# Performance work log

Hardware: AMD Instinct MI355X
Metric: run time of the kernel (lower is better)

## Reference

```python
import jax, jax.numpy as jnp
import numpy as np

B, L, DIM, HEADS, DIM_HEAD = 16, 1024, 512, 8, 64


def _make_perms(rng):
    # perm = identity on first DIM indices, random permutation of [DIM, L*DIM) after
    perms = []
    for _ in range(HEADS - 1):
        tail = rng.permutation(np.arange(DIM, L * DIM))
        perms.append(np.concatenate([np.arange(DIM), tail]))
    return jnp.asarray(np.stack(perms), dtype=jnp.int64)


def setup_inputs() -> dict:
    key = jax.random.key(0)
    ks = jax.random.split(key, 6)
    s = 0.02
    return {
        "x": jax.random.normal(ks[0], (B, L, DIM), dtype=jnp.float32),
        "perms": _make_perms(np.random.default_rng(0)),
        "Wq": jax.random.normal(ks[1], (HEADS, DIM, DIM_HEAD), dtype=jnp.float32) * s,
        "Wk": jax.random.normal(ks[2], (HEADS, DIM, DIM_HEAD), dtype=jnp.float32) * s,
        "Wv": jax.random.normal(ks[3], (HEADS, DIM, DIM_HEAD), dtype=jnp.float32) * s,
        "Wo": jax.random.normal(ks[4], (DIM, HEADS * DIM_HEAD), dtype=jnp.float32) * s,
        "bo": jnp.zeros((DIM,), dtype=jnp.float32),
    }


def reference(x, perms, Wq, Wk, Wv, Wo, bo):
    b, l, d = x.shape
    h, _, e = Wq.shape
    scale = e ** -0.5
    # shuffled query inputs for heads 1..h-1
    flat = x.reshape(b, l * d)                      # [B, L*D]
    shuf = flat[:, perms].reshape(b, h - 1, l, d)   # [B, H-1, L, D]
    xq = jnp.concatenate([x[:, None], shuf], axis=1)  # [B, H, L, D]
    q = jnp.einsum('bhld,hde->bhle', xq, Wq)
    k = jnp.einsum('bld,hde->bhle', x, Wk)
    v = jnp.einsum('bld,hde->bhle', x, Wv)
    attn = jax.nn.softmax(jnp.einsum('bhqe,bhke->bhqk', q, k) * scale, axis=-1)
    out = jnp.einsum('bhqk,bhke->bhqe', attn, v)    # [B, H, L, E]
    out = out.transpose(0, 2, 1, 3).reshape(b, l, h * e)  # concat heads on last dim
    return jnp.einsum('bli,di->bld', out, Wo) + bo
```

## Files before the change

### kernel.cpp

```cpp
#include <hip/hip_runtime.h>

#define LL 1024
#define DD 512
#define HH 8
#define EE 64
#define LDX (LL*DD)
#define BB 16

typedef _Float16 h8 __attribute__((ext_vector_type(8)));
typedef _Float16 h4 __attribute__((ext_vector_type(4)));
typedef float f4 __attribute__((ext_vector_type(4)));
typedef int i4 __attribute__((ext_vector_type(4)));

__device__ __forceinline__ f4 mfma16(h8 a, h8 b, f4 c) {
    return __builtin_amdgcn_mfma_f32_16x16x32_f16(a, b, c, 0, 0, 0);
}

__global__ __launch_bounds__(256) void k_prep(
    const float* __restrict__ x, _Float16* __restrict__ xT)
{
    const int s = blockIdx.x * 256 + threadIdx.x;
    h8 lo, hi;
    #pragma unroll
    for (int b = 0; b < 8; ++b)  lo[b] = (_Float16)x[(size_t)b*LDX + s];
    #pragma unroll
    for (int b = 0; b < 8; ++b)  hi[b] = (_Float16)x[(size_t)(b+8)*LDX + s];
    _Float16* d = xT + (size_t)s * BB;
    *(h8*)d = lo; *(h8*)(d + 8) = hi;
}

__global__ __launch_bounds__(256) void k_x16(
    const float* __restrict__ x, _Float16* __restrict__ x16)
{
    const int i = blockIdx.x * 256 + threadIdx.x;
    f4 v = ((const f4*)x)[i];
    h4 o;
    #pragma unroll
    for (int j = 0; j < 4; ++j) o[j] = (_Float16)v[j];
    *(h4*)(x16 + 4*(size_t)i) = o;
}

__global__ __launch_bounds__(256) void k_wprep(
    const float* __restrict__ Wq, const float* __restrict__ Wk,
    const float* __restrict__ Wv, _Float16* __restrict__ WT)
{
    const int d0 = blockIdx.x * 64;
    const int zz = blockIdx.y;
    const float* src; float sc = 1.f;
    if (zz < 8)       src = Wk + (size_t)zz*DD*EE;
    else if (zz < 16) src = Wv + (size_t)(zz-8)*DD*EE;
    else            { src = Wq + (size_t)(zz-16)*DD*EE; sc = 0.125f; }
    const int t = threadIdx.x;
    const int e = t & 63, dq = t >> 6;
    #pragma unroll
    for (int i = 0; i < 16; ++i) {
        int d = d0 + dq*16 + i;
        WT[(size_t)(zz*64 + e)*DD + d] = (_Float16)(src[(size_t)d*EE + e] * sc);
    }
}

__global__ __launch_bounds__(256) void k_wo16(
    const float* __restrict__ Wo, _Float16* __restrict__ Wo16)
{
    const int i = blockIdx.x * 256 + threadIdx.x;
    f4 v = ((const f4*)Wo)[i];
    #pragma unroll
    for (int j = 0; j < 4; ++j) Wo16[4*i + j] = (_Float16)v[j];
}

__global__ __launch_bounds__(256) void k_qkv(
    const _Float16* __restrict__ x16, const _Float16* __restrict__ WT,
    _Float16* __restrict__ qw, _Float16* __restrict__ kw, _Float16* __restrict__ vw)
{
    const int y  = blockIdx.x;
    const int r0 = blockIdx.y * 128;

    __shared__ __align__(16) _Float16 As[2][128][72];
    __shared__ __align__(16) _Float16 Bs[2][128][72];

    const int t = threadIdx.x;
    const int wv = t >> 6, lane = t & 63;
    const int m = lane & 15, qd = lane >> 4;
    const int sr = t >> 1, sc0 = (t & 1) * 32;

    const _Float16* ax = x16 + (size_t)(r0 + sr)*DD + sc0;
    const _Float16* bx = WT  + (size_t)(y*128 + sr)*DD + sc0;

    #pragma unroll
    for (int c = 0; c < 4; ++c) {
        *(h8*)&As[0][sr][sc0 + 8*c] = *(const h8*)(ax + 8*c);
        *(h8*)&Bs[0][sr][sc0 + 8*c] = *(const h8*)(bx + 8*c);
    }
    __syncthreads();

    f4 acc[2][8] = {};
    int cur = 0;
    for (int kt = 0; kt < 8; ++kt) {
        const int alt = cur ^ 1;
        h8 an[4], bn[4];
        if (kt < 7) {
            const _Float16* a2 = ax + (kt+1)*64;
            const _Float16* b2 = bx + (kt+1)*64;
            #pragma unroll
            for (int c = 0; c < 4; ++c) {
                an[c] = *(const h8*)(a2 + 8*c);
                bn[c] = *(const h8*)(b2 + 8*c);
            }
        }
        #pragma unroll
        for (int ks = 0; ks < 2; ++ks) {
            h8 a0 = *(const h8*)&As[cur][32*wv +  0 + m][32*ks + 8*qd];
            h8 a1 = *(const h8*)&As[cur][32*wv + 16 + m][32*ks + 8*qd];
            #pragma unroll
            for (int nt = 0; nt < 8; ++nt) {
                h8 bb = *(const h8*)&Bs[cur][16*nt + m][32*ks + 8*qd];
                acc[0][nt] = mfma16(a0, bb, acc[0][nt]);
                acc[1][nt] = mfma16(a1, bb, acc[1][nt]);
            }
        }
        if (kt < 7) {
            #pragma unroll
            for (int c = 0; c < 4; ++c) {
                *(h8*)&As[alt][sr][sc0 + 8*c] = an[c];
                *(h8*)&Bs[alt][sr][sc0 + 8*c] = bn[c];
            }
            __syncthreads();
            cur = alt;
        }
    }

    #pragma unroll
    for (int nt = 0; nt < 8; ++nt) {
        const int n = y*128 + 16*nt + m;
        const int z = n >> 6, e = n & 63;
        if (z >= 17) continue;
        _Float16* dst; int h;
        if (z < 8)       { dst = kw; h = z; }
        else if (z < 16) { dst = vw; h = z - 8; }
        else             { dst = qw; h = 0; }
        dst += (size_t)h*LL*EE + e;
        #pragma unroll
        for (int mt = 0; mt < 2; ++mt)
            #pragma unroll
            for (int r = 0; r < 4; ++r) {
                int R = r0 + 32*wv + 16*mt + 4*qd + r;
                int b = R >> 10, l = R & 1023;
                dst[((size_t)b*HH*LL + l)*EE] = (_Float16)acc[mt][nt][r];
            }
    }
}

__global__ __launch_bounds__(256) void k_qshuf(
    const _Float16* __restrict__ xT, const int* __restrict__ perms,
    const _Float16* __restrict__ WT, _Float16* __restrict__ qw)
{
    const int l0 = blockIdx.x * 4;
    const int h  = blockIdx.y + 1;
    const _Float16* Wb = WT + (size_t)((16 + h)*64)*DD;
    const int* pbase = perms + (size_t)(h-1)*LDX;

    __shared__ __align__(16) _Float16 As[2][64][72];
    __shared__ __align__(16) _Float16 Bs[2][64][72];

    const int t = threadIdx.x;
    const int wv = t >> 6, lane = t & 63;
    const int m = lane & 15, qd = lane >> 4;
    const int lg = t >> 6, kcol = t & 63;
    const int br = t >> 2, bc0 = (t & 3) * 16;

    int pv[8];
    #pragma unroll
    for (int kt = 0; kt < 8; ++kt)
        pv[kt] = pbase[(size_t)(l0 + lg)*DD + kt*64 + kcol];

    {
        const _Float16* g = xT + (size_t)pv[0] * BB;
        h8 g0 = *(const h8*)g, g1 = *(const h8*)(g + 8);
        const _Float16* s = Wb + (size_t)br*DD + bc0;
        *(h8*)&Bs[0][br][bc0]     = *(const h8*)s;
        *(h8*)&Bs[0][br][bc0 + 8] = *(const h8*)(s + 8);
        #pragma unroll
        for (int i = 0; i < 8; ++i) As[0][lg*16 + i][kcol]     = g0[i];
        #pragma unroll
        for (int i = 0; i < 8; ++i) As[0][lg*16 + 8 + i][kcol] = g1[i];
    }
    __syncthreads();

    f4 acc[4] = {};
    int cur = 0;
    for (int kt = 0; kt < 8; ++kt) {
        const int alt = cur ^ 1;
        h8 g0n, g1n, b0n, b1n;
        if (kt < 7) {
            const _Float16* g = xT + (size_t)pv[kt+1] * BB;
            g0n = *(const h8*)g; g1n = *(const h8*)(g + 8);
            const _Float16* s = Wb + (size_t)br*DD + (kt+1)*64 + bc0;
            b0n = *(const h8*)s; b1n = *(const h8*)(s + 8);
        }
        #pragma unroll
        for (int ks = 0; ks < 2; ++ks) {
            h8 a = *(const h8*)&As[cur][16*wv + m][32*ks + 8*qd];
            #pragma unroll
            for (int nt = 0; nt < 4; ++nt) {
                h8 bb = *(const h8*)&Bs[cur][16*nt + m][32*ks + 8*qd];
                acc[nt] = mfma16(a, bb, acc[nt]);
            }
        }
        if (kt < 7) {
            *(h8*)&Bs[alt][br][bc0]     = b0n;
            *(h8*)&Bs[alt][br][bc0 + 8] = b1n;
            #pragma unroll
            for (int i = 0; i < 8; ++i) As[alt][lg*16 + i][kcol]     = g0n[i];
            #pragma unroll
            for (int i = 0; i < 8; ++i) As[alt][lg*16 + 8 + i][kcol] = g1n[i];
            __syncthreads();
            cur = alt;
        }
    }
    #pragma unroll
    for (int nt = 0; nt < 4; ++nt)
        #pragma unroll
        for (int r = 0; r < 4; ++r) {
            int b = 4*qd + r;
            qw[((size_t)(b*HH + h)*LL + l0 + wv)*EE + 16*nt + m] = (_Float16)acc[nt][r];
        }
}

__global__ __launch_bounds__(256, 3) void k_attn(
    const _Float16* __restrict__ qw, const _Float16* __restrict__ kw,
    const _Float16* __restrict__ vw, _Float16* __restrict__ oa)
{
    const int bh = blockIdx.x;
    const int l0 = blockIdx.y * 128;
    const int b = bh >> 3, h = bh & 7;
    const _Float16* qb = qw + ((size_t)bh*LL + l0)*EE;
    const _Float16* kb = kw + (size_t)bh*LL*EE;
    const _Float16* vb = vw + (size_t)bh*LL*EE;

    __shared__ __align__(16) _Float16 KsF[2][64*64];
    __shared__ __align__(16) _Float16 VtsF[2][64*64];
    __shared__ __align__(16) _Float16 Ps[128][72];

    const int t = threadIdx.x;
    const int wv = t >> 6, lane = t & 63;
    const int m = lane & 15, qd = lane >> 4;
    const int m7 = m & 7;
    const int krow = t >> 2, c0 = t & 3;
    const int vkey = t & 63, vec = t >> 6;
    const int vhi = vkey >> 3, vlo = vkey & 7;

    h8 qa[2][2];
    #pragma unroll
    for (int mt = 0; mt < 2; ++mt)
        #pragma unroll
        for (int ks = 0; ks < 2; ++ks)
            qa[mt][ks] = *(const h8*)(qb + (size_t)(32*wv + 16*mt + m)*EE + 32*ks + 8*qd);

    f4 oacc[2][4] = {};
    float lp[2][4] = {};

    {
        const _Float16* sk = kb + (size_t)krow*EE + 16*c0;
        h8 k0 = *(const h8*)sk, k1 = *(const h8*)(sk + 8);
        const _Float16* sv = vb + (size_t)vkey*EE + 16*vec;
        h8 v0 = *(const h8*)sv, v1 = *(const h8*)(sv + 8);
        *(h8*)&KsF[0][(krow<<6) + 8*((2*c0)     ^ (krow & 7))] = k0;
        *(h8*)&KsF[0][(krow<<6) + 8*((2*c0 + 1) ^ (krow & 7))] = k1;
        #pragma unroll
        for (int i = 0; i < 8; ++i)
            VtsF[0][((16*vec + i)<<6)     + 8*(vhi ^ i) + vlo] = v0[i];
        #pragma unroll
        for (int i = 0; i < 8; ++i)
            VtsF[0][((16*vec + 8 + i)<<6) + 8*(vhi ^ i) + vlo] = v1[i];
    }
    __syncthreads();

    for (int kt = 0; kt < 16; ++kt) {
        const int cur = kt & 1, alt = cur ^ 1;
        h8 kn0, kn1, vn0, vn1;
        if (kt < 15) {
            const _Float16* sk = kb + (size_t)((kt+1)*64 + krow)*EE + 16*c0;
            kn0 = *(const h8*)sk; kn1 = *(const h8*)(sk + 8);
            const _Float16* sv = vb + (size_t)((kt+1)*64 + vkey)*EE + 16*vec;
            vn0 = *(const h8*)sv; vn1 = *(const h8*)(sv + 8);
        }
        f4 sacc[2][4] = {};
        #pragma unroll
        for (int ks = 0; ks < 2; ++ks)
            #pragma unroll
            for (int nt = 0; nt < 4; ++nt) {
                h8 kf = *(const h8*)&KsF[cur][((16*nt + m)<<6) + 8*((4*ks + qd) ^ m7)];
                sacc[0][nt] = mfma16(qa[0][ks], kf, sacc[0][nt]);
                sacc[1][nt] = mfma16(qa[1][ks], kf, sacc[1][nt]);
            }
        #pragma unroll
        for (int mt = 0; mt < 2; ++mt)
            #pragma unroll
            for (int nt = 0; nt < 4; ++nt)
                #pragma unroll
                for (int r = 0; r < 4; ++r) {
                    float e = __expf(sacc[mt][nt][r]);
                    lp[mt][r] += e;
                    Ps[32*wv + 16*mt + 4*qd + r][16*nt + m] = (_Float16)e;
                }
        #pragma unroll
        for (int ks = 0; ks < 2; ++ks) {
            h8 pa0 = *(const h8*)&Ps[32*wv +  0 + m][32*ks + 8*qd];
            h8 pa1 = *(const h8*)&Ps[32*wv + 16 + m][32*ks + 8*qd];
            #pragma unroll
            for (int nt = 0; nt < 4; ++nt) {
                h8 vf = *(const h8*)&VtsF[cur][((16*nt + m)<<6) + 8*((4*ks + qd) ^ m7)];
                oacc[0][nt] = mfma16(pa0, vf, oacc[0][nt]);
                oacc[1][nt] = mfma16(pa1, vf, oacc[1][nt]);
            }
        }
        if (kt < 15) {
            *(h8*)&KsF[alt][(krow<<6) + 8*((2*c0)     ^ (krow & 7))] = kn0;
            *(h8*)&KsF[alt][(krow<<6) + 8*((2*c0 + 1) ^ (krow & 7))] = kn1;
            #pragma unroll
            for (int i = 0; i < 8; ++i)
                VtsF[alt][((16*vec + i)<<6)     + 8*(vhi ^ i) + vlo] = vn0[i];
            #pragma unroll
            for (int i = 0; i < 8; ++i)
                VtsF[alt][((16*vec + 8 + i)<<6) + 8*(vhi ^ i) + vlo] = vn1[i];
            __syncthreads();
        }
    }

    #pragma unroll
    for (int mt = 0; mt < 2; ++mt)
        #pragma unroll
        for (int r = 0; r < 4; ++r) {
            float s = lp[mt][r];
            s += __shfl_xor(s, 1, 64);
            s += __shfl_xor(s, 2, 64);
            s += __shfl_xor(s, 4, 64);
            s += __shfl_xor(s, 8, 64);
            lp[mt][r] = s;
        }

    _Float16* ob = oa + ((size_t)(b*LL + l0))*(HH*EE) + h*EE;
    #pragma unroll
    for (int mt = 0; mt < 2; ++mt)
        #pragma unroll
        for (int nt = 0; nt < 4; ++nt)
            #pragma unroll
            for (int r = 0; r < 4; ++r) {
                int row = 32*wv + 16*mt + 4*qd + r;
                ob[(size_t)row*(HH*EE) + 16*nt + m] = (_Float16)(oacc[mt][nt][r] / lp[mt][r]);
            }
}

__global__ __launch_bounds__(256) void k_oproj(
    const _Float16* __restrict__ oa, const _Float16* __restrict__ Wo16,
    const float* __restrict__ bo, float* __restrict__ out)
{
    const int y  = blockIdx.x;
    const int r0 = blockIdx.y * 128;

    __shared__ __align__(16) _Float16 As[2][128][72];
    __shared__ __align__(16) _Float16 Bs[2][128][72];

    const int t = threadIdx.x;
    const int wv = t >> 6, lane = t & 63;
    const int m = lane & 15, qd = lane >> 4;
    const int sr = t >> 1, sc0 = (t & 1) * 32;

    const _Float16* ax = oa   + (size_t)(r0 + sr)*DD + sc0;
    const _Float16* bx = Wo16 + (size_t)(y*128 + sr)*DD + sc0;

    #pragma unroll
    for (int c = 0; c < 4; ++c) {
        *(h8*)&As[0][sr][sc0 + 8*c] = *(const h8*)(ax + 8*c);
        *(h8*)&Bs[0][sr][sc0 + 8*c] = *(const h8*)(bx + 8*c);
    }
    __syncthreads();

    f4 acc[2][8] = {};
    int cur = 0;
    for (int kt = 0; kt < 8; ++kt) {
        const int alt = cur ^ 1;
        h8 an[4], bn[4];
        if (kt < 7) {
            const _Float16* a2 = ax + (kt+1)*64;
            const _Float16* b2 = bx + (kt+1)*64;
            #pragma unroll
            for (int c = 0; c < 4; ++c) {
                an[c] = *(const h8*)(a2 + 8*c);
                bn[c] = *(const h8*)(b2 + 8*c);
            }
        }
        #pragma unroll
        for (int ks = 0; ks < 2; ++ks) {
            h8 a0 = *(const h8*)&As[cur][32*wv +  0 + m][32*ks + 8*qd];
            h8 a1 = *(const h8*)&As[cur][32*wv + 16 + m][32*ks + 8*qd];
            #pragma unroll
            for (int nt = 0; nt < 8; ++nt) {
                h8 bb = *(const h8*)&Bs[cur][16*nt + m][32*ks + 8*qd];
                acc[0][nt] = mfma16(a0, bb, acc[0][nt]);
                acc[1][nt] = mfma16(a1, bb, acc[1][nt]);
            }
        }
        if (kt < 7) {
            #pragma unroll
            for (int c = 0; c < 4; ++c) {
                *(h8*)&As[alt][sr][sc0 + 8*c] = an[c];
                *(h8*)&Bs[alt][sr][sc0 + 8*c] = bn[c];
            }
            __syncthreads();
            cur = alt;
        }
    }

    #pragma unroll
    for (int nt = 0; nt < 8; ++nt) {
        const int col = y*128 + 16*nt + m;
        const float bias = bo[col];
        #pragma unroll
        for (int mt = 0; mt < 2; ++mt)
            #pragma unroll
            for (int r = 0; r < 4; ++r) {
                int row = 32*wv + 16*mt + 4*qd + r;
                out[(size_t)(r0 + row)*DD + col] = acc[mt][nt][r] + bias;
            }
    }
}

extern "C" void kernel_launch(void* const* d_in, const int* in_sizes, int n_in,
                              void* d_out, int out_size, void* d_ws, size_t ws_size,
                              hipStream_t stream)
{
    const float* x  = (const float*)d_in[0];
    const int*   pm = (const int*)d_in[1];
    const float* Wq = (const float*)d_in[2];
    const float* Wk = (const float*)d_in[3];
    const float* Wv = (const float*)d_in[4];
    const float* Wo = (const float*)d_in[5];
    const float* bo = (const float*)d_in[6];
    float* out = (float*)d_out;

    const size_t QS = (size_t)BB * HH * LL * EE;
    _Float16* q    = (_Float16*)d_ws;
    _Float16* k    = q + QS;
    _Float16* v    = k + QS;
    _Float16* oaw  = v + QS;
    _Float16* xT   = oaw;
    _Float16* WT   = oaw + QS;
    _Float16* Wo16 = WT + (size_t)24*64*DD;
    _Float16* x16  = (_Float16*)d_out;

    k_x16  <<<dim3(LDX*BB/1024),    256, 0, stream>>>(x, x16);
    k_prep <<<dim3(LDX/256),        256, 0, stream>>>(x, xT);
    k_wprep<<<dim3(8, 24),          256, 0, stream>>>(Wq, Wk, Wv, WT);
    k_wo16 <<<dim3(DD*DD/1024),     256, 0, stream>>>(Wo, Wo16);
    k_qkv  <<<dim3(9, BB*LL/128),   256, 0, stream>>>(x16, WT, q, k, v);
    k_qshuf<<<dim3(LL/4, HH-1),     256, 0, stream>>>(xT, pm, WT, q);
    k_attn <<<dim3(BB*HH, LL/128),  256, 0, stream>>>(q, k, v, oaw);
    k_oproj<<<dim3(DD/128, BB*LL/128), 256, 0, stream>>>(oaw, Wo16, bo, out);
}
```

Measured before the change: 290.1 us.

## Keep softmax probabilities in registers via transposed QK^T and permlane swaps

The attention kernel now computes S^T by swapping the MFMA operands, so the exp2 results sit in registers in a layout that permlane16_swap can repack into the A operand of the PV MFMA. This removes the shared-memory round trip for P and the Ps buffer. Row sums are taken with an extra MFMA against a ones vector instead of shuffle reductions. The Q scale folds in log2(e) so the cheaper exp2 can be used, and the final divide becomes a reciprocal multiply. The occupancy hint rises from 3 to 4 blocks per CU, which tightens the register budget and could cause spills; the round-toward-zero fp16 packing also slightly changes numerics.

New measurement: 278.8 us. 3.9% less time.

```diff
diff --git a/kernel.cpp b/kernel.cpp
--- a/kernel.cpp
+++ b/kernel.cpp
@@ -49,7 +49,7 @@
     const float* src; float sc = 1.f;
     if (zz < 8)       src = Wk + (size_t)zz*DD*EE;
     else if (zz < 16) src = Wv + (size_t)(zz-8)*DD*EE;
-    else            { src = Wq + (size_t)(zz-16)*DD*EE; sc = 0.125f; }
+    else            { src = Wq + (size_t)(zz-16)*DD*EE; sc = 0.18033688011112042f; }
     const int t = threadIdx.x;
     const int e = t & 63, dq = t >> 6;
     #pragma unroll
@@ -226,7 +226,7 @@
         }
 }
 
-__global__ __launch_bounds__(256, 3) void k_attn(
+__global__ __launch_bounds__(256, 4) void k_attn(
     const _Float16* __restrict__ qw, const _Float16* __restrict__ kw,
     const _Float16* __restrict__ vw, _Float16* __restrict__ oa)
 {
@@ -239,12 +239,12 @@
 
     __shared__ __align__(16) _Float16 KsF[2][64*64];
     __shared__ __align__(16) _Float16 VtsF[2][64*64];
-    __shared__ __align__(16) _Float16 Ps[128][72];
 
     const int t = threadIdx.x;
     const int wv = t >> 6, lane = t & 63;
     const int m = lane & 15, qd = lane >> 4;
     const int m7 = m & 7;
+    const int qdp = ((qd & 1) << 1) | (qd >> 1);
     const int krow = t >> 2, c0 = t & 3;
     const int vkey = t & 63, vec = t >> 6;
     const int vhi = vkey >> 3, vlo = vkey & 7;
@@ -257,7 +257,10 @@
             qa[mt][ks] = *(const h8*)(qb + (size_t)(32*wv + 16*mt + m)*EE + 32*ks + 8*qd);
 
     f4 oacc[2][4] = {};
-    float lp[2][4] = {};
+    f4 lpacc[2] = {};
+    h8 ones;
+    #pragma unroll
+    for (int i = 0; i < 8; ++i) ones[i] = (_Float16)1.f;
 
     {
         const _Float16* sk = kb + (size_t)krow*EE + 16*c0;
@@ -284,36 +287,54 @@
             const _Float16* sv = vb + (size_t)((kt+1)*64 + vkey)*EE + 16*vec;
             vn0 = *(const h8*)sv; vn1 = *(const h8*)(sv + 8);
         }
+
         f4 sacc[2][4] = {};
         #pragma unroll
         for (int ks = 0; ks < 2; ++ks)
             #pragma unroll
             for (int nt = 0; nt < 4; ++nt) {
                 h8 kf = *(const h8*)&KsF[cur][((16*nt + m)<<6) + 8*((4*ks + qd) ^ m7)];
-                sacc[0][nt] = mfma16(qa[0][ks], kf, sacc[0][nt]);
-                sacc[1][nt] = mfma16(qa[1][ks], kf, sacc[1][nt]);
-            }
+                sacc[0][nt] = mfma16(kf, qa[0][ks], sacc[0][nt]);
+                sacc[1][nt] = mfma16(kf, qa[1][ks], sacc[1][nt]);
+            }
+
+        unsigned E[2][4][2];
         #pragma unroll
         for (int mt = 0; mt < 2; ++mt)
             #pragma unroll
-            for (int nt = 0; nt < 4; ++nt)
-                #pragma unroll
-                for (int r = 0; r < 4; ++r) {
-                    float e = __expf(sacc[mt][nt][r]);
-                    lp[mt][r] += e;
-                    Ps[32*wv + 16*mt + 4*qd + r][16*nt + m] = (_Float16)e;
-                }
+            for (int nt = 0; nt < 4; ++nt) {
+                float e0 = __builtin_amdgcn_exp2f(sacc[mt][nt][0]);
+                float e1 = __builtin_amdgcn_exp2f(sacc[mt][nt][1]);
+                float e2 = __builtin_amdgcn_exp2f(sacc[mt][nt][2]);
+                float e3 = __builtin_amdgcn_exp2f(sacc[mt][nt][3]);
+                E[mt][nt][0] = __builtin_bit_cast(unsigned, __builtin_amdgcn_cvt_pkrtz(e0, e1));
+                E[mt][nt][1] = __builtin_bit_cast(unsigned, __builtin_amdgcn_cvt_pkrtz(e2, e3));
+            }
+
+        h8 pa[2][2];
+        #pragma unroll
+        for (int mt = 0; mt < 2; ++mt)
+            #pragma unroll
+            for (int ks = 0; ks < 2; ++ks) {
+                auto x = __builtin_amdgcn_permlane16_swap(E[mt][2*ks][0], E[mt][2*ks+1][0], false, false);
+                auto y = __builtin_amdgcn_permlane16_swap(E[mt][2*ks][1], E[mt][2*ks+1][1], false, false);
+                i4 pw;
+                pw[0] = (int)x[0]; pw[1] = (int)y[0]; pw[2] = (int)x[1]; pw[3] = (int)y[1];
+                pa[mt][ks] = __builtin_bit_cast(h8, pw);
+            }
+
         #pragma unroll
         for (int ks = 0; ks < 2; ++ks) {
-            h8 pa0 = *(const h8*)&Ps[32*wv +  0 + m][32*ks + 8*qd];
-            h8 pa1 = *(const h8*)&Ps[32*wv + 16 + m][32*ks + 8*qd];
             #pragma unroll
             for (int nt = 0; nt < 4; ++nt) {
-                h8 vf = *(const h8*)&VtsF[cur][((16*nt + m)<<6) + 8*((4*ks + qd) ^ m7)];
-                oacc[0][nt] = mfma16(pa0, vf, oacc[0][nt]);
-                oacc[1][nt] = mfma16(pa1, vf, oacc[1][nt]);
-            }
-        }
+                h8 vf = *(const h8*)&VtsF[cur][((16*nt + m)<<6) + 8*((4*ks + qdp) ^ m7)];
+                oacc[0][nt] = mfma16(pa[0][ks], vf, oacc[0][nt]);
+                oacc[1][nt] = mfma16(pa[1][ks], vf, oacc[1][nt]);
+            }
+            lpacc[0] = mfma16(pa[0][ks], ones, lpacc[0]);
+            lpacc[1] = mfma16(pa[1][ks], ones, lpacc[1]);
+        }
+
         if (kt < 15) {
             *(h8*)&KsF[alt][(krow<<6) + 8*((2*c0)     ^ (krow & 7))] = kn0;
             *(h8*)&KsF[alt][(krow<<6) + 8*((2*c0 + 1) ^ (krow & 7))] = kn1;
@@ -327,28 +348,18 @@
         }
     }
 
+    _Float16* ob = oa + ((size_t)(b*LL + l0))*(HH*EE) + h*EE;
     #pragma unroll
     for (int mt = 0; mt < 2; ++mt)
         #pragma unroll
         for (int r = 0; r < 4; ++r) {
-            float s = lp[mt][r];
-            s += __shfl_xor(s, 1, 64);
-            s += __shfl_xor(s, 2, 64);
-            s += __shfl_xor(s, 4, 64);
-            s += __shfl_xor(s, 8, 64);
-            lp[mt][r] = s;
-        }
-
-    _Float16* ob = oa + ((size_t)(b*LL + l0))*(HH*EE) + h*EE;
-    #pragma unroll
-    for (int mt = 0; mt < 2; ++mt)
-        #pragma unroll
-        for (int nt = 0; nt < 4; ++nt)
-            #pragma unroll
-            for (int r = 0; r < 4; ++r) {
+            const float inv = __builtin_amdgcn_rcpf(lpacc[mt][r]);
+            #pragma unroll
+            for (int nt = 0; nt < 4; ++nt) {
                 int row = 32*wv + 16*mt + 4*qd + r;
-                ob[(size_t)row*(HH*EE) + 16*nt + m] = (_Float16)(oacc[mt][nt][r] / lp[mt][r]);
-            }
+                ob[(size_t)row*(HH*EE) + 16*nt + m] = (_Float16)(oacc[mt][nt][r] * inv);
+            }
+        }
 }
 
 __global__ __launch_bounds__(256) void k_oproj(
```
